# Optimization experiments

Hardware: AMD Instinct MI355X
Metric: run time of the kernel (lower is better)

The kernel has to match this reference:

```python
import jax, jax.numpy as jnp
import numpy as np

N = 50000      # total atoms in batched graph
E = 800000     # edges
IN = 128       # in_feats
OUT = 64       # out_feats (per GAT head)
H = 4          # num_heads
NEG_SLOPE = 0.2
BN_EPS = 1e-5


def setup_inputs() -> dict:
    key = jax.random.key(0)
    ks = jax.random.split(key, 16)
    s = 0.1  # keep activations well-scaled
    return {
        "node_feats": jax.random.normal(ks[0], (N, IN), jnp.float32),
        "W_fc":       jax.random.normal(ks[1], (IN, H * OUT), jnp.float32) * s,
        "attn_l":     jax.random.normal(ks[2], (H, OUT), jnp.float32) * s,
        "attn_r":     jax.random.normal(ks[3], (H, OUT), jnp.float32) * s,
        "gat_res_w":  jax.random.normal(ks[4], (IN, H * OUT), jnp.float32) * s,
        "gat_bias":   jax.random.normal(ks[5], (H * OUT,), jnp.float32) * s,
        "conv_w":     jax.random.normal(ks[6], (1, H, 1), jnp.float32) * s,
        "conv_b":     jax.random.normal(ks[7], (1,), jnp.float32) * s,
        "res_w":      jax.random.normal(ks[8], (IN, OUT), jnp.float32) * s,
        "res_b":      jax.random.normal(ks[9], (OUT,), jnp.float32) * s,
        "bn_gamma":   jnp.ones((OUT,), jnp.float32),
        "bn_beta":    jnp.zeros((OUT,), jnp.float32),
        "src":        jax.random.randint(ks[10], (E,), 0, N, jnp.int32),
        "dst":        jax.random.randint(ks[11], (E,), 0, N, jnp.int32),
        "etype":      0,
    }


def reference(node_feats, W_fc, attn_l, attn_r, gat_res_w, gat_bias,
              conv_w, conv_b, res_w, res_b, bn_gamma, bn_beta,
              src, dst, etype):
    # ---- GATConv (DGL semantics, eval mode: no dropout) ----
    h = (node_feats @ W_fc).reshape(-1, H, OUT)            # [N,H,D]
    el = jnp.sum(h * attn_l, axis=-1)                      # [N,H]
    er = jnp.sum(h * attn_r, axis=-1)                      # [N,H]
    e = jax.nn.leaky_relu(el[src] + er[dst], NEG_SLOPE)    # [E,H]
    # segment softmax over incoming edges of each dst node
    m = jax.ops.segment_max(e, dst, num_segments=N)        # [N,H]
    m = jnp.where(jnp.isfinite(m), m, 0.0)                 # empty segments
    a = jnp.exp(e - m[dst])                                # [E,H]
    ssum = jax.ops.segment_sum(a, dst, num_segments=N)     # [N,H]
    alpha = a / (ssum[dst] + 1e-16)                        # [E,H]
    # weighted aggregation: rst[v] = sum_{(u->v)} alpha * h[u]
    rst = jax.ops.segment_sum(alpha[:, :, None] * h[src], dst, num_segments=N)  # [N,H,D]
    # GAT residual (in != H*OUT -> linear res_fc, no bias) + bias + activation
    rst = rst + (node_feats @ gat_res_w).reshape(-1, H, OUT) + gat_bias.reshape(H, OUT)
    rst = jax.nn.relu(rst)                                 # [N,H,D]
    # ---- Conv1d(4 -> 1, kernel=1): weighted head merge ----
    y = jnp.einsum("nhd,h->nd", rst, conv_w[0, :, 0]) + conv_b[0]  # [N,D]
    # ---- outer residual ----
    y = y + jax.nn.relu(node_feats @ res_w + res_b)
    # ---- BatchNorm1d (training-style batch stats) ----
    mean = jnp.mean(y, axis=0)
    var = jnp.var(y, axis=0)
    return (y - mean) / jnp.sqrt(var + BN_EPS) * bn_gamma + bn_beta
```

## Files before the change

kernel.cpp:

```cpp
#include <hip/hip_runtime.h>

#define IN_F   128
#define OUTD   64
#define HOUT   256
#define NEG_SLOPE 0.2f
#define BN_EPS 1e-5f
#define NCOLS  592
#define K1_BLOCKS 512
#define K1_TOTWAVES (K1_BLOCKS * 4)

typedef __attribute__((ext_vector_type(8))) short bf16x8;
typedef __attribute__((ext_vector_type(4))) float f32x4;
typedef __attribute__((ext_vector_type(2))) float f32x2;

__device__ __forceinline__ unsigned short f2bf(float f) {
    union { float f; unsigned u; } v; v.f = f;
    unsigned r = (v.u + 0x7FFF + ((v.u >> 16) & 1)) >> 16;
    return (unsigned short)r;
}
__device__ __forceinline__ float bf2f(unsigned short h) {
    union { unsigned u; float f; } v; v.u = ((unsigned)h) << 16;
    return v.f;
}

__device__ __forceinline__ int b2idx(int c, int k) {
    int n = c >> 6, j = (c >> 4) & 3, n15 = c & 15;
    int ks = k >> 5, qd = (k >> 3) & 3, kk = k & 7;
    return ((((n * 4 + j) * 4 + ks) * 64) + qd * 16 + n15) * 8 + kk;
}

__global__ __launch_bounds__(256) void k0_pack(
    const float* __restrict__ W_fc, const float* __restrict__ W_gres,
    const float* __restrict__ W_res,
    const float* __restrict__ attn_l, const float* __restrict__ attn_r,
    unsigned short* __restrict__ Btg2)
{
    int bid = blockIdx.x, t = threadIdx.x;
    if (bid < 288) {
        int idx = bid * 256 + t;
        int c = idx >> 7, k = idx & 127;
        float v;
        if (c < 256)      v = W_fc[k * HOUT + c];
        else if (c < 512) v = W_gres[k * HOUT + (c - 256)];
        else              v = W_res[k * OUTD + (c - 512)];
        Btg2[b2idx(c, k)] = f2bf(v);
        return;
    }
    for (int p = t; p < 512; p += 256) {
        int h = p >> 7, k = p & 127;
        float sl = 0.f, sr = 0.f;
        for (int d = 0; d < 64; ++d) {
            float wv = W_fc[k * HOUT + h * 64 + d];
            sl += wv * attn_l[h * 64 + d];
            sr += wv * attn_r[h * 64 + d];
        }
        Btg2[b2idx(576 + h, k)] = f2bf(sl);
        Btg2[b2idx(580 + h, k)] = f2bf(sr);
    }
    for (int p = t; p < 8 * 128; p += 256) {
        int c = 584 + (p >> 7), k = p & 127;
        Btg2[b2idx(c, k)] = 0;
    }
}

__global__ __launch_bounds__(256) void k1_gemm(
    const float* __restrict__ A, const unsigned short* __restrict__ Btg2,
    const float* __restrict__ gat_bias, const float* __restrict__ res_b,
    const int* __restrict__ dst, int* __restrict__ degree, int* __restrict__ rank,
    unsigned char* __restrict__ Hh8, unsigned char* __restrict__ Hr8,
    unsigned short* __restrict__ Rres,
    float* __restrict__ el, float* __restrict__ er,
    int N, int E)
{
    int t = threadIdx.x;
    int w = t >> 6, lane = t & 63, quad = lane >> 4, n15 = lane & 15;
    int gw = blockIdx.x * 4 + w;
    int T = (N + 31) / 32;

    if (gw < T) {
        int m0 = gw * 32;

        bf16x8 af[2][4];
#pragma unroll
        for (int i = 0; i < 2; ++i) {
            int r = m0 + i * 16 + n15;
#pragma unroll
            for (int ks = 0; ks < 4; ++ks) {
                float4 v0 = make_float4(0.f, 0.f, 0.f, 0.f), v1 = v0;
                if (r < N) {
                    const float* ap = A + (size_t)r * IN_F + ks * 32 + quad * 8;
                    v0 = *(const float4*)ap;
                    v1 = *(const float4*)(ap + 4);
                }
                bf16x8 o;
                o[0] = f2bf(v0.x); o[1] = f2bf(v0.y); o[2] = f2bf(v0.z); o[3] = f2bf(v0.w);
                o[4] = f2bf(v1.x); o[5] = f2bf(v1.y); o[6] = f2bf(v1.z); o[7] = f2bf(v1.w);
                af[i][ks] = o;
            }
        }

        float gbv[4][4], rbv[4];
#pragma unroll
        for (int hd = 0; hd < 4; ++hd)
#pragma unroll
            for (int j = 0; j < 4; ++j) gbv[hd][j] = gat_bias[hd * 64 + j * 16 + n15];
#pragma unroll
        for (int j = 0; j < 4; ++j) rbv[j] = res_b[j * 16 + n15];

        unsigned hpack[2][4][4] = {};
        unsigned rpack[2][4][4] = {};
        int lofs = (quad * 16 + n15) * 8;

        for (int n = 0; n < 9; ++n) {
            f32x4 acc[2][4] = {};
#pragma unroll
            for (int ks = 0; ks < 4; ++ks) {
                bf16x8 bfr[4];
#pragma unroll
                for (int j = 0; j < 4; ++j)
                    bfr[j] = *(const bf16x8*)(Btg2 + (((n * 4 + j) * 4 + ks) << 9) + lofs);
#pragma unroll
                for (int i = 0; i < 2; ++i)
#pragma unroll
                    for (int j = 0; j < 4; ++j)
                        acc[i][j] = __builtin_amdgcn_mfma_f32_16x16x32_bf16(af[i][ks], bfr[j], acc[i][j], 0, 0, 0);
            }
            if (n < 4) {
#pragma unroll
                for (int i = 0; i < 2; ++i)
#pragma unroll
                    for (int j = 0; j < 4; ++j)
#pragma unroll
                        for (int reg = 0; reg < 4; ++reg) {
                            float v = acc[i][j][reg];
                            unsigned pk = (unsigned)__builtin_amdgcn_cvt_pk_fp8_f32(v, v, 0, false);
                            hpack[i][j][reg] |= (pk & 0xffu) << (8 * n);
                        }
            } else if (n < 8) {
                int hd = n - 4;
#pragma unroll
                for (int i = 0; i < 2; ++i)
#pragma unroll
                    for (int j = 0; j < 4; ++j)
#pragma unroll
                        for (int reg = 0; reg < 4; ++reg) {
                            float v = acc[i][j][reg] + gbv[hd][j];
                            unsigned pk = (unsigned)__builtin_amdgcn_cvt_pk_fp8_f32(v, v, 0, false);
                            rpack[i][j][reg] |= (pk & 0xffu) << (8 * hd);
                        }
            } else {
#pragma unroll
                for (int i = 0; i < 2; ++i)
#pragma unroll
                    for (int reg = 0; reg < 4; ++reg) {
                        int r = m0 + i * 16 + quad * 4 + reg;
                        if (r < N) {
#pragma unroll
                            for (int j = 0; j < 4; ++j)
                                Rres[(size_t)r * OUTD + j * 16 + n15] = f2bf(acc[i][j][reg] + rbv[j]);
                        }
                    }
            }
        }

        f32x4 acc2[2] = {};
#pragma unroll
        for (int ks = 0; ks < 4; ++ks) {
            bf16x8 b = *(const bf16x8*)(Btg2 + (((9 * 4 + 0) * 4 + ks) << 9) + lofs);
            acc2[0] = __builtin_amdgcn_mfma_f32_16x16x32_bf16(af[0][ks], b, acc2[0], 0, 0, 0);
            acc2[1] = __builtin_amdgcn_mfma_f32_16x16x32_bf16(af[1][ks], b, acc2[1], 0, 0, 0);
        }
#pragma unroll
        for (int i = 0; i < 2; ++i)
#pragma unroll
            for (int reg = 0; reg < 4; ++reg) {
                int r = m0 + i * 16 + quad * 4 + reg;
                if (r < N && n15 < 8) {
                    float v = acc2[i][reg];
                    if (n15 < 4) el[(size_t)r * 4 + n15] = v;
                    else         er[(size_t)r * 4 + (n15 - 4)] = v;
                }
            }

#pragma unroll
        for (int i = 0; i < 2; ++i)
#pragma unroll
            for (int reg = 0; reg < 4; ++reg) {
                int r = m0 + i * 16 + quad * 4 + reg;
                if (r < N) {
#pragma unroll
                    for (int j = 0; j < 4; ++j) {
                        *(unsigned*)(Hh8 + ((size_t)r << 8) + (j * 16 + n15) * 4) = hpack[i][j][reg];
                        *(unsigned*)(Hr8 + ((size_t)r << 8) + (j * 16 + n15) * 4) = rpack[i][j][reg];
                    }
                }
            }
    }

    for (int e = gw * 64 + lane; e < E; e += K1_TOTWAVES * 64)
        rank[e] = atomicAdd(degree + dst[e], 1);
}

__global__ __launch_bounds__(256) void scanA_kernel(const int* __restrict__ degree,
                                                    int* __restrict__ excl,
                                                    int* __restrict__ blocksum, int N) {
    __shared__ int sm[256];
    int t = threadIdx.x;
    int i = blockIdx.x * 256 + t;
    int d = (i < N) ? degree[i] : 0;
    sm[t] = d; __syncthreads();
    for (int off = 1; off < 256; off <<= 1) {
        int v = (t >= off) ? sm[t - off] : 0;
        __syncthreads();
        sm[t] += v;
        __syncthreads();
    }
    if (i < N) excl[i] = sm[t] - d;
    if (t == 255) blocksum[blockIdx.x] = sm[255];
}

__global__ __launch_bounds__(256) void scanB_kernel(const int* __restrict__ blocksum,
                                                    int* __restrict__ base, int nb) {
    __shared__ int sm[256];
    int t = threadIdx.x;
    int d = (t < nb) ? blocksum[t] : 0;
    sm[t] = d; __syncthreads();
    for (int off = 1; off < 256; off <<= 1) {
        int v = (t >= off) ? sm[t - off] : 0;
        __syncthreads();
        sm[t] += v;
        __syncthreads();
    }
    if (t < nb) base[t] = sm[t] - d;
}

__global__ void scatter_kernel(const int* __restrict__ src, const int* __restrict__ dst,
                               const int* __restrict__ rank, const int* __restrict__ excl,
                               const int* __restrict__ base,
                               const float* __restrict__ el, const float* __restrict__ er,
                               uint4* __restrict__ es_sorted, int E) {
    int e = blockIdx.x * 256 + threadIdx.x;
    if (e >= E) return;
    int d = dst[e], u = src[e];
    int p = excl[d] + base[d >> 8] + rank[e];
    float4 l = *(const float4*)(el + (size_t)u * 4);
    float4 r = *(const float4*)(er + (size_t)d * 4);
    float x, s0, s1, s2, s3;
    x = l.x + r.x; x = x > 0.f ? x : NEG_SLOPE * x; s0 = __expf(x);
    x = l.y + r.y; x = x > 0.f ? x : NEG_SLOPE * x; s1 = __expf(x);
    x = l.z + r.z; x = x > 0.f ? x : NEG_SLOPE * x; s2 = __expf(x);
    x = l.w + r.w; x = x > 0.f ? x : NEG_SLOPE * x; s3 = __expf(x);
    uint4 o;
    o.x = (unsigned)u << 8;
    o.y = (unsigned)f2bf(s0) | ((unsigned)f2bf(s1) << 16);
    o.z = (unsigned)f2bf(s2) | ((unsigned)f2bf(s3) << 16);
    o.w = 0u;
    es_sorted[p] = o;
}

__global__ __launch_bounds__(256) void agg_kernel(
    const unsigned char* __restrict__ Hh8, const unsigned char* __restrict__ Hr8,
    const unsigned short* __restrict__ Rres,
    const int* __restrict__ excl, const int* __restrict__ base,
    const uint4* __restrict__ es_sorted,
    const float* __restrict__ conv_w, const float* __restrict__ conv_b,
    float* __restrict__ y, int N, int E)
{
    int wave = threadIdx.x >> 6, lane = threadIdx.x & 63;
    int v = blockIdx.x * 4 + wave;
    if (v >= N) return;
    int b  = excl[v] + base[v >> 8];
    int e2 = (v + 1 < N) ? (excl[v + 1] + base[(v + 1) >> 8]) : E;
    int deg = e2 - b;

    const unsigned char* hbase = Hh8 + lane * 4;
    float a0 = 0.f, a1 = 0.f, a2 = 0.f, a3 = 0.f;
    float p0 = 0.f, p1 = 0.f, p2 = 0.f, p3 = 0.f;

    for (int i0 = 0; i0 < deg; i0 += 64) {
        int j = i0 + lane;
        uint4 es = make_uint4(0u, 0u, 0u, 0u);
        if (j < deg) es = es_sorted[b + j];
        p0 += bf2f((unsigned short)(es.y & 0xffff));
        p1 += bf2f((unsigned short)(es.y >> 16));
        p2 += bf2f((unsigned short)(es.z & 0xffff));
        p3 += bf2f((unsigned short)(es.z >> 16));
        int cl = deg - i0; if (cl > 64) cl = 64;
        int jj = 0;
        for (; jj + 1 < cl; jj += 2) {
            unsigned uA   = (unsigned)__builtin_amdgcn_readlane((int)es.x, jj);
            unsigned sA01 = (unsigned)__builtin_amdgcn_readlane((int)es.y, jj);
            unsigned sA23 = (unsigned)__builtin_amdgcn_readlane((int)es.z, jj);
            unsigned uB   = (unsigned)__builtin_amdgcn_readlane((int)es.x, jj + 1);
            unsigned sB01 = (unsigned)__builtin_amdgcn_readlane((int)es.y, jj + 1);
            unsigned sB23 = (unsigned)__builtin_amdgcn_readlane((int)es.z, jj + 1);
            unsigned hvA = *(const unsigned*)(hbase + uA);
            unsigned hvB = *(const unsigned*)(hbase + uB);
            f32x2 loA = __builtin_amdgcn_cvt_pk_f32_fp8(hvA, false);
            f32x2 hiA = __builtin_amdgcn_cvt_pk_f32_fp8(hvA, true);
            f32x2 loB = __builtin_amdgcn_cvt_pk_f32_fp8(hvB, false);
            f32x2 hiB = __builtin_amdgcn_cvt_pk_f32_fp8(hvB, true);
            a0 += bf2f((unsigned short)(sA01 & 0xffff)) * loA.x;
            a1 += bf2f((unsigned short)(sA01 >> 16))    * loA.y;
            a2 += bf2f((unsigned short)(sA23 & 0xffff)) * hiA.x;
            a3 += bf2f((unsigned short)(sA23 >> 16))    * hiA.y;
            a0 += bf2f((unsigned short)(sB01 & 0xffff)) * loB.x;
            a1 += bf2f((unsigned short)(sB01 >> 16))    * loB.y;
            a2 += bf2f((unsigned short)(sB23 & 0xffff)) * hiB.x;
            a3 += bf2f((unsigned short)(sB23 >> 16))    * hiB.y;
        }
        if (jj < cl) {
            unsigned uA   = (unsigned)__builtin_amdgcn_readlane((int)es.x, jj);
            unsigned sA01 = (unsigned)__builtin_amdgcn_readlane((int)es.y, jj);
            unsigned sA23 = (unsigned)__builtin_amdgcn_readlane((int)es.z, jj);
            unsigned hvA = *(const unsigned*)(hbase + uA);
            f32x2 loA = __builtin_amdgcn_cvt_pk_f32_fp8(hvA, false);
            f32x2 hiA = __builtin_amdgcn_cvt_pk_f32_fp8(hvA, true);
            a0 += bf2f((unsigned short)(sA01 & 0xffff)) * loA.x;
            a1 += bf2f((unsigned short)(sA01 >> 16))    * loA.y;
            a2 += bf2f((unsigned short)(sA23 & 0xffff)) * hiA.x;
            a3 += bf2f((unsigned short)(sA23 >> 16))    * hiA.y;
        }
    }
#pragma unroll
    for (int off = 1; off < 64; off <<= 1) {
        p0 += __shfl_xor(p0, off); p1 += __shfl_xor(p1, off);
        p2 += __shfl_xor(p2, off); p3 += __shfl_xor(p3, off);
    }
    float r0 = 1.f / (p0 + 1e-16f), r1 = 1.f / (p1 + 1e-16f);
    float r2 = 1.f / (p2 + 1e-16f), r3 = 1.f / (p3 + 1e-16f);

    unsigned hr = *(const unsigned*)(Hr8 + ((size_t)v << 8) + lane * 4);
    f32x2 rlo = __builtin_amdgcn_cvt_pk_f32_fp8(hr, false);
    f32x2 rhi = __builtin_amdgcn_cvt_pk_f32_fp8(hr, true);
    float resv = bf2f(Rres[(size_t)v * OUTD + lane]);
    float yv = conv_b[0] + (resv > 0.f ? resv : 0.f);
    float tt;
    tt = a0 * r0 + rlo.x; tt = tt > 0.f ? tt : 0.f; yv += conv_w[0] * tt;
    tt = a1 * r1 + rlo.y; tt = tt > 0.f ? tt : 0.f; yv += conv_w[1] * tt;
    tt = a2 * r2 + rhi.x; tt = tt > 0.f ? tt : 0.f; yv += conv_w[2] * tt;
    tt = a3 * r3 + rhi.y; tt = tt > 0.f ? tt : 0.f; yv += conv_w[3] * tt;
    y[(size_t)v * OUTD + lane] = yv;
}

__global__ __launch_bounds__(256) void bn_partial_kernel(const float* __restrict__ y,
                                                         float* __restrict__ bnsum,
                                                         float* __restrict__ bnsumsq, int total) {
    __shared__ float smem[256];
    int t = threadIdx.x;
    size_t idx = (size_t)blockIdx.x * 256 + t;
    size_t stride = (size_t)gridDim.x * 256;
    float sum = 0.f, sq = 0.f;
    for (; idx < (size_t)total; idx += stride) {
        float v = y[idx];
        sum += v; sq += v * v;
    }
    int d = t & 63;
    smem[t] = sum; __syncthreads();
    if (t < 64) atomicAdd(bnsum + d, smem[t] + smem[t + 64] + smem[t + 128] + smem[t + 192]);
    __syncthreads();
    smem[t] = sq; __syncthreads();
    if (t < 64) atomicAdd(bnsumsq + d, smem[t] + smem[t + 64] + smem[t + 128] + smem[t + 192]);
}

__global__ void norm_kernel(const float* __restrict__ y,
                            const float* __restrict__ bnsum, const float* __restrict__ bnsumsq,
                            const float* __restrict__ gamma, const float* __restrict__ beta,
                            float* __restrict__ out, int total4, float invN) {
    int idx = blockIdx.x * blockDim.x + threadIdx.x;
    if (idx >= total4) return;
    float4 v = *(const float4*)(y + (size_t)idx * 4);
    int d = (idx * 4) & 63;
    float4 o;
#pragma unroll
    for (int k = 0; k < 4; ++k) {
        float mean = bnsum[d + k] * invN;
        float var = bnsumsq[d + k] * invN - mean * mean;
        float sc = gamma[d + k] * rsqrtf(var + BN_EPS);
        float sh = beta[d + k] - mean * sc;
        (&o.x)[k] = (&v.x)[k] * sc + sh;
    }
    *(float4*)(out + (size_t)idx * 4) = o;
}

extern "C" void kernel_launch(void* const* d_in, const int* in_sizes, int n_in,
                              void* d_out, int out_size, void* d_ws, size_t ws_size,
                              hipStream_t stream) {
    const float* node_feats = (const float*)d_in[0];
    const float* W_fc       = (const float*)d_in[1];
    const float* attn_l     = (const float*)d_in[2];
    const float* attn_r     = (const float*)d_in[3];
    const float* gat_res_w  = (const float*)d_in[4];
    const float* gat_bias   = (const float*)d_in[5];
    const float* conv_w     = (const float*)d_in[6];
    const float* conv_b     = (const float*)d_in[7];
    const float* res_w      = (const float*)d_in[8];
    const float* res_b      = (const float*)d_in[9];
    const float* bn_gamma   = (const float*)d_in[10];
    const float* bn_beta    = (const float*)d_in[11];
    const int*   src        = (const int*)d_in[12];
    const int*   dst        = (const int*)d_in[13];

    const int N = in_sizes[0] / IN_F;
    const int E = in_sizes[12];
    const int nb = (N + 255) / 256;

    char* ws = (char*)d_ws;
    size_t off = 0;
    auto alloc = [&](size_t bytes) -> void* {
        void* p = (void*)(ws + off);
        off += (bytes + 255) & ~(size_t)255;
        return p;
    };

    int*   degree  = (int*)alloc((size_t)N * 4);
    float* bnsum   = (float*)alloc(64 * 4);
    float* bnsumsq = (float*)alloc(64 * 4);
    size_t zero_bytes = off;
    int*            rank      = (int*)alloc((size_t)E * 4);
    int*            excl      = (int*)alloc((size_t)N * 4);
    int*            blocksum  = (int*)alloc(256 * 4);
    int*            base      = (int*)alloc(256 * 4);
    uint4*          es_sorted = (uint4*)alloc((size_t)E * 16);
    unsigned short* Btg2      = (unsigned short*)alloc((size_t)NCOLS * IN_F * 2);
    unsigned char*  Hh8       = (unsigned char*)alloc((size_t)N * 256);
    unsigned char*  Hr8       = (unsigned char*)alloc((size_t)N * 256);
    unsigned short* Rres      = (unsigned short*)alloc((size_t)N * OUTD * 2);
    float*          el        = (float*)alloc((size_t)N * 4 * 4);
    float*          er        = (float*)alloc((size_t)N * 4 * 4);
    float*          y         = (float*)alloc((size_t)N * OUTD * 4);
    (void)ws_size; (void)n_in; (void)out_size;

    hipMemsetAsync(d_ws, 0, zero_bytes, stream);

    k0_pack<<<289, 256, 0, stream>>>(W_fc, gat_res_w, res_w, attn_l, attn_r, Btg2);
    k1_gemm<<<K1_BLOCKS, 256, 0, stream>>>(node_feats, Btg2, gat_bias, res_b,
                                           dst, degree, rank, Hh8, Hr8, Rres,
                                           el, er, N, E);
    scanA_kernel<<<nb, 256, 0, stream>>>(degree, excl, blocksum, N);
    scanB_kernel<<<1, 256, 0, stream>>>(blocksum, base, nb);
    scatter_kernel<<<(E + 255) / 256, 256, 0, stream>>>(src, dst, rank, excl, base,
                                                        el, er, es_sorted, E);
    agg_kernel<<<(N + 3) / 4, 256, 0, stream>>>(Hh8, Hr8, Rres, excl, base, es_sorted,
                                                conv_w, conv_b, y, N, E);
    bn_partial_kernel<<<512, 256, 0, stream>>>(y, bnsum, bnsumsq, N * OUTD);
    norm_kernel<<<(N * OUTD / 4 + 255) / 256, 256, 0, stream>>>(y, bnsum, bnsumsq,
                                                                bn_gamma, bn_beta, (float*)d_out,
                                                                N * OUTD / 4, 1.f / (float)N);
}
```

Before: 258.7 us.

## Restructure GEMM column tiling to pack fp8 per head-group and cut register pressure

```diff
diff --git a/kernel.cpp b/kernel.cpp
--- a/kernel.cpp
+++ b/kernel.cpp
@@ -5,8 +5,7 @@
 #define HOUT   256
 #define NEG_SLOPE 0.2f
 #define BN_EPS 1e-5f
-#define NCOLS  592
-#define K1_BLOCKS 512
+#define K1_BLOCKS 768
 #define K1_TOTWAVES (K1_BLOCKS * 4)
 
 typedef __attribute__((ext_vector_type(8))) short bf16x8;
@@ -24,9 +23,14 @@
 }
 
 __device__ __forceinline__ int b2idx(int c, int k) {
-    int n = c >> 6, j = (c >> 4) & 3, n15 = c & 15;
+    int tt, j;
+    if (c < 256)      { tt = (c >> 4) & 3;                     j = c >> 6; }
+    else if (c < 512) { int cc = c - 256; tt = 4 + ((cc >> 4) & 3); j = cc >> 6; }
+    else if (c < 576) { int cc = c - 512; tt = 8;              j = cc >> 4; }
+    else              { tt = 9;                                j = 0; }
+    int n15 = c & 15;
     int ks = k >> 5, qd = (k >> 3) & 3, kk = k & 7;
-    return ((((n * 4 + j) * 4 + ks) * 64) + qd * 16 + n15) * 8 + kk;
+    return ((((tt * 4 + j) * 4 + ks) * 64) + qd * 16 + n15) * 8 + kk;
 }
 
 __global__ __launch_bounds__(256) void k0_pack(
@@ -77,8 +81,8 @@
     int gw = blockIdx.x * 4 + w;
     int T = (N + 31) / 32;
 
-    if (gw < T) {
-        int m0 = gw * 32;
+    for (int task = gw; task < T; task += K1_TOTWAVES) {
+        int m0 = task * 32;
 
         bf16x8 af[2][4];
 #pragma unroll
@@ -99,102 +103,115 @@
             }
         }
 
-        float gbv[4][4], rbv[4];
-#pragma unroll
-        for (int hd = 0; hd < 4; ++hd)
-#pragma unroll
-            for (int j = 0; j < 4; ++j) gbv[hd][j] = gat_bias[hd * 64 + j * 16 + n15];
-#pragma unroll
-        for (int j = 0; j < 4; ++j) rbv[j] = res_b[j * 16 + n15];
-
-        unsigned hpack[2][4][4] = {};
-        unsigned rpack[2][4][4] = {};
         int lofs = (quad * 16 + n15) * 8;
 
-        for (int n = 0; n < 9; ++n) {
+#pragma unroll 2
+        for (int s = 0; s < 4; ++s) {
             f32x4 acc[2][4] = {};
 #pragma unroll
             for (int ks = 0; ks < 4; ++ks) {
                 bf16x8 bfr[4];
 #pragma unroll
                 for (int j = 0; j < 4; ++j)
-                    bfr[j] = *(const bf16x8*)(Btg2 + (((n * 4 + j) * 4 + ks) << 9) + lofs);
+                    bfr[j] = *(const bf16x8*)(Btg2 + ((s * 16 + j * 4 + ks) << 9) + lofs);
 #pragma unroll
                 for (int i = 0; i < 2; ++i)
 #pragma unroll
                     for (int j = 0; j < 4; ++j)
                         acc[i][j] = __builtin_amdgcn_mfma_f32_16x16x32_bf16(af[i][ks], bfr[j], acc[i][j], 0, 0, 0);
             }
-            if (n < 4) {
-#pragma unroll
-                for (int i = 0; i < 2; ++i)
-#pragma unroll
-                    for (int j = 0; j < 4; ++j)
-#pragma unroll
-                        for (int reg = 0; reg < 4; ++reg) {
-                            float v = acc[i][j][reg];
-                            unsigned pk = (unsigned)__builtin_amdgcn_cvt_pk_fp8_f32(v, v, 0, false);
-                            hpack[i][j][reg] |= (pk & 0xffu) << (8 * n);
-                        }
-            } else if (n < 8) {
-                int hd = n - 4;
-#pragma unroll
-                for (int i = 0; i < 2; ++i)
-#pragma unroll
-                    for (int j = 0; j < 4; ++j)
-#pragma unroll
-                        for (int reg = 0; reg < 4; ++reg) {
-                            float v = acc[i][j][reg] + gbv[hd][j];
-                            unsigned pk = (unsigned)__builtin_amdgcn_cvt_pk_fp8_f32(v, v, 0, false);
-                            rpack[i][j][reg] |= (pk & 0xffu) << (8 * hd);
-                        }
-            } else {
-#pragma unroll
-                for (int i = 0; i < 2; ++i)
-#pragma unroll
-                    for (int reg = 0; reg < 4; ++reg) {
-                        int r = m0 + i * 16 + quad * 4 + reg;
-                        if (r < N) {
-#pragma unroll
-                            for (int j = 0; j < 4; ++j)
-                                Rres[(size_t)r * OUTD + j * 16 + n15] = f2bf(acc[i][j][reg] + rbv[j]);
-                        }
-                    }
-            }
-        }
-
-        f32x4 acc2[2] = {};
-#pragma unroll
-        for (int ks = 0; ks < 4; ++ks) {
-            bf16x8 b = *(const bf16x8*)(Btg2 + (((9 * 4 + 0) * 4 + ks) << 9) + lofs);
-            acc2[0] = __builtin_amdgcn_mfma_f32_16x16x32_bf16(af[0][ks], b, acc2[0], 0, 0, 0);
-            acc2[1] = __builtin_amdgcn_mfma_f32_16x16x32_bf16(af[1][ks], b, acc2[1], 0, 0, 0);
-        }
-#pragma unroll
-        for (int i = 0; i < 2; ++i)
-#pragma unroll
-            for (int reg = 0; reg < 4; ++reg) {
-                int r = m0 + i * 16 + quad * 4 + reg;
-                if (r < N && n15 < 8) {
-                    float v = acc2[i][reg];
-                    if (n15 < 4) el[(size_t)r * 4 + n15] = v;
-                    else         er[(size_t)r * 4 + (n15 - 4)] = v;
-                }
-            }
-
-#pragma unroll
-        for (int i = 0; i < 2; ++i)
-#pragma unroll
-            for (int reg = 0; reg < 4; ++reg) {
-                int r = m0 + i * 16 + quad * 4 + reg;
-                if (r < N) {
-#pragma unroll
-                    for (int j = 0; j < 4; ++j) {
-                        *(unsigned*)(Hh8 + ((size_t)r << 8) + (j * 16 + n15) * 4) = hpack[i][j][reg];
-                        *(unsigned*)(Hr8 + ((size_t)r << 8) + (j * 16 + n15) * 4) = rpack[i][j][reg];
+#pragma unroll
+            for (int i = 0; i < 2; ++i)
+#pragma unroll
+                for (int reg = 0; reg < 4; ++reg) {
+                    int r = m0 + i * 16 + quad * 4 + reg;
+                    if (r < N) {
+                        unsigned pk = (unsigned)__builtin_amdgcn_cvt_pk_fp8_f32(acc[i][0][reg], acc[i][1][reg], 0, false);
+                        pk = (unsigned)__builtin_amdgcn_cvt_pk_fp8_f32(acc[i][2][reg], acc[i][3][reg], (int)pk, true);
+                        *(unsigned*)(Hh8 + ((size_t)r << 8) + (s * 16 + n15) * 4) = pk;
                     }
                 }
+        }
+
+#pragma unroll 2
+        for (int s = 0; s < 4; ++s) {
+            f32x4 acc[2][4] = {};
+#pragma unroll
+            for (int ks = 0; ks < 4; ++ks) {
+                bf16x8 bfr[4];
+#pragma unroll
+                for (int j = 0; j < 4; ++j)
+                    bfr[j] = *(const bf16x8*)(Btg2 + (((4 + s) * 16 + j * 4 + ks) << 9) + lofs);
+#pragma unroll
+                for (int i = 0; i < 2; ++i)
+#pragma unroll
+                    for (int j = 0; j < 4; ++j)
+                        acc[i][j] = __builtin_amdgcn_mfma_f32_16x16x32_bf16(af[i][ks], bfr[j], acc[i][j], 0, 0, 0);
             }
+            float b0 = gat_bias[0 * 64 + s * 16 + n15];
+            float b1 = gat_bias[1 * 64 + s * 16 + n15];
+            float b2 = gat_bias[2 * 64 + s * 16 + n15];
+            float b3 = gat_bias[3 * 64 + s * 16 + n15];
+#pragma unroll
+            for (int i = 0; i < 2; ++i)
+#pragma unroll
+                for (int reg = 0; reg < 4; ++reg) {
+                    int r = m0 + i * 16 + quad * 4 + reg;
+                    if (r < N) {
+                        unsigned pk = (unsigned)__builtin_amdgcn_cvt_pk_fp8_f32(acc[i][0][reg] + b0, acc[i][1][reg] + b1, 0, false);
+                        pk = (unsigned)__builtin_amdgcn_cvt_pk_fp8_f32(acc[i][2][reg] + b2, acc[i][3][reg] + b3, (int)pk, true);
+                        *(unsigned*)(Hr8 + ((size_t)r << 8) + (s * 16 + n15) * 4) = pk;
+                    }
+                }
+        }
+
+        {
+            f32x4 acc[2][4] = {};
+#pragma unroll
+            for (int ks = 0; ks < 4; ++ks) {
+                bf16x8 bfr[4];
+#pragma unroll
+                for (int j = 0; j < 4; ++j)
+                    bfr[j] = *(const bf16x8*)(Btg2 + ((8 * 16 + j * 4 + ks) << 9) + lofs);
+#pragma unroll
+                for (int i = 0; i < 2; ++i)
+#pragma unroll
+                    for (int j = 0; j < 4; ++j)
+                        acc[i][j] = __builtin_amdgcn_mfma_f32_16x16x32_bf16(af[i][ks], bfr[j], acc[i][j], 0, 0, 0);
+            }
+#pragma unroll
+            for (int i = 0; i < 2; ++i)
+#pragma unroll
+                for (int reg = 0; reg < 4; ++reg) {
+                    int r = m0 + i * 16 + quad * 4 + reg;
+                    if (r < N) {
+#pragma unroll
+                        for (int j = 0; j < 4; ++j)
+                            Rres[(size_t)r * OUTD + j * 16 + n15] = f2bf(acc[i][j][reg] + res_b[j * 16 + n15]);
+                    }
+                }
+        }
+
+        {
+            f32x4 acc2[2] = {};
+#pragma unroll
+            for (int ks = 0; ks < 4; ++ks) {
+                bf16x8 b = *(const bf16x8*)(Btg2 + ((9 * 16 + ks) << 9) + lofs);
+                acc2[0] = __builtin_amdgcn_mfma_f32_16x16x32_bf16(af[0][ks], b, acc2[0], 0, 0, 0);
+                acc2[1] = __builtin_amdgcn_mfma_f32_16x16x32_bf16(af[1][ks], b, acc2[1], 0, 0, 0);
+            }
+#pragma unroll
+            for (int i = 0; i < 2; ++i)
+#pragma unroll
+                for (int reg = 0; reg < 4; ++reg) {
+                    int r = m0 + i * 16 + quad * 4 + reg;
+                    if (r < N && n15 < 8) {
+                        float v = acc2[i][reg];
+                        if (n15 < 4) el[(size_t)r * 4 + n15] = v;
+                        else         er[(size_t)r * 4 + (n15 - 4)] = v;
+                    }
+                }
+        }
     }
 
     for (int e = gw * 64 + lane; e < E; e += K1_TOTWAVES * 64)
@@ -422,7 +439,7 @@
     int*            blocksum  = (int*)alloc(256 * 4);
     int*            base      = (int*)alloc(256 * 4);
     uint4*          es_sorted = (uint4*)alloc((size_t)E * 16);
-    unsigned short* Btg2      = (unsigned short*)alloc((size_t)NCOLS * IN_F * 2);
+    unsigned short* Btg2      = (unsigned short*)alloc((size_t)10 * 16 * 512 * 2);
     unsigned char*  Hh8       = (unsigned char*)alloc((size_t)N * 256);
     unsigned char*  Hr8       = (unsigned char*)alloc((size_t)N * 256);
     unsigned short* Rres      = (unsigned short*)alloc((size_t)N * OUTD * 2);
```

After: 261.8 us. Within noise of the previous version (+1.2%).
